# Performance work log

Hardware: AMD Instinct MI355X
Metric: run time of the kernel (lower is better)

The kernel has to match this reference:

```python
import jax, jax.numpy as jnp
import numpy as np

N_BONES = 8
NV = 14062
PARENTS = [-1, 0, 1, 2, 3, 4, 5, 6]  # kinematic chain


def rotvec_to_rotmat(rv):
    # rv: [..., 3] -> [..., 3, 3] via Rodrigues
    ang = jnp.sqrt(jnp.sum(rv * rv, axis=-1) + 1e-12)  # [...]
    k = rv / ang[..., None]
    kx, ky, kz = k[..., 0], k[..., 1], k[..., 2]
    z = jnp.zeros_like(kx)
    K = jnp.stack([
        jnp.stack([z, -kz, ky], -1),
        jnp.stack([kz, z, -kx], -1),
        jnp.stack([-ky, kx, z], -1)], -2)  # [...,3,3]
    s = jnp.sin(ang)[..., None, None]
    c = jnp.cos(ang)[..., None, None]
    I = jnp.eye(3, dtype=rv.dtype)
    return I + s * K + (1.0 - c) * (K @ K)


def bilinear_sample(img, gx, gy):
    # img: [H, W]; gx, gy: [B, Nv] normalized coords in [-1,1]
    # bilinear, border padding, align_corners=True (matches F.grid_sample)
    H, W = img.shape
    x = jnp.clip((gx + 1.0) * 0.5 * (W - 1), 0.0, W - 1.0)
    y = jnp.clip((gy + 1.0) * 0.5 * (H - 1), 0.0, H - 1.0)
    x0 = jnp.floor(x); y0 = jnp.floor(y)
    x0i = x0.astype(jnp.int32); y0i = y0.astype(jnp.int32)
    x1i = jnp.minimum(x0i + 1, W - 1); y1i = jnp.minimum(y0i + 1, H - 1)
    wx = x - x0; wy = y - y0
    v00 = img[y0i, x0i]; v01 = img[y0i, x1i]
    v10 = img[y1i, x0i]; v11 = img[y1i, x1i]
    return (v00 * (1 - wx) + v01 * wx) * (1 - wy) + (v10 * (1 - wx) + v11 * wx) * wy


def setup_inputs() -> dict:
    key = jax.random.key(0)
    ks = jax.random.split(key, 12)
    B = 256
    theta = jax.random.normal(ks[0], (B, N_BONES, 3), jnp.float32) * 0.3
    tau = jax.random.normal(ks[1], (B, 1), jnp.float32) * 0.1
    alpha = jax.random.uniform(ks[2], (B, 1), jnp.float32)
    bsw = jax.random.uniform(ks[3], (B, 55), jnp.float32)
    W = jax.random.uniform(ks[4], (N_BONES, NV), jnp.float32) + 1e-3
    W = W / W.sum(axis=0, keepdims=True)  # done in HACK.__init__
    T = jax.random.normal(ks[5], (NV, 3), jnp.float32)
    P = jax.random.normal(ks[6], (N_BONES, 3, 3, NV, 3), jnp.float32) * 0.01
    L = jax.random.uniform(ks[7], (1, 1, 256, 256), jnp.float32)
    ts = jax.random.normal(ks[8], (NV, 3), jnp.float32)
    # L2P: per-bone rigid transforms (rotation + small translation)
    rv = jax.random.normal(ks[9], (N_BONES, 3), jnp.float32) * 0.2
    R = rotvec_to_rotmat(rv)
    t = jax.random.normal(ks[10], (N_BONES, 3), jnp.float32) * 0.1
    L2P = jnp.tile(jnp.eye(4, dtype=jnp.float32), (N_BONES, 1, 1))
    L2P = L2P.at[:, :3, :3].set(R).at[:, :3, 3].set(t)
    E = jax.random.normal(ks[11], (55, NV, 3), jnp.float32) * 0.05
    uvgrid = jax.random.uniform(jax.random.fold_in(key, 99), (NV, 2), jnp.float32)
    return {"theta": theta, "tau": tau, "alpha": alpha, "bsw": bsw, "W": W,
            "T": T, "P": P, "L": L, "ts": ts, "L2P": L2P, "E": E, "uvgrid": uvgrid}


def reference(theta, tau, alpha, bsw, W, T, P, L, ts, L2P, E, uvgrid):
    B = theta.shape[0]
    R = rotvec_to_rotmat(theta)  # [B, Nb, 3, 3]
    # theta_matrix_zero: bone 0 subtracts itself (-> 0), others subtract I
    sub = jnp.concatenate([R[:, :1],
                           jnp.broadcast_to(jnp.eye(3, dtype=R.dtype), (B, N_BONES - 1, 3, 3))], axis=1)
    theta_zero = R - sub  # [B, Nb, 3, 3]
    # pose-corrective blendshapes: sum over (bone, i, j)
    P_theta = jnp.einsum('bnij,nijvk->bvk', theta_zero, P)  # [B, Nv, 3]

    # forward kinematics along chain: L2W_pose[i] = L2W_pose[parent] @ (L2P[i] @ local[i])
    local = jnp.tile(jnp.eye(4, dtype=R.dtype), (B, N_BONES, 1, 1))
    local = local.at[:, :, :3, :3].set(R)  # [B, Nb, 4, 4]
    mats = []
    for i in range(N_BONES):
        Ai = jnp.einsum('ij,bjk->bik', L2P[i], local[:, i])
        if PARENTS[i] >= 0:
            Ai = jnp.matmul(mats[PARENTS[i]], Ai)
        mats.append(Ai)
    L2W_pose = jnp.stack(mats, axis=1)  # [B, Nb, 4, 4]

    # rest-pose world-to-local (inverse bind matrices)
    rest = []
    for i in range(N_BONES):
        rest.append(L2P[i] if PARENTS[i] < 0 else rest[PARENTS[i]] @ L2P[i])
    W2L = jnp.linalg.inv(jnp.stack(rest))  # [Nb, 4, 4]

    W2L2pWs = jnp.einsum('bnij,njk->bnik', L2W_pose, W2L)  # [B, Nb, 4, 4]
    # skinning-weight contraction over bones -> per-vertex 4x4 transform
    M = jnp.einsum('bnij,nv->bvij', W2L2pWs, W)  # [B, Nv, 4, 4]

    # larynx displacement via grid_sample
    uv = uvgrid * 2.0 - 1.0  # [Nv, 2]
    gx = jnp.broadcast_to(uv[None, :, 0], (B, uv.shape[0]))
    gy = uv[None, :, 1] + tau * 2.0  # shift y by tau*2 (F.pad(tau*2,[1,0]))
    dist = bilinear_sample(L[0, 0], gx, gy)  # [B, Nv]
    L_tau = dist[:, :, None] * ts[None]  # [B, Nv, 3]

    T_theta = (T[None] + P_theta
               + jnp.einsum('bn,nvk->bvk', bsw, E)
               + L_tau * alpha[:, :, None])  # [B, Nv, 3]

    # homogeneous per-vertex 4x4 matvec, keep xyz
    T_transformed = (jnp.einsum('bvij,bvj->bvi', M[:, :, :3, :3], T_theta)
                     + M[:, :, :3, 3])
    return T_transformed
```

## Files before the change

kernel.cpp:

```cpp
#include <hip/hip_runtime.h>
#include <cmath>

#define NB     8
#define NVERT  14062
#define NV3    42186
#define BATCH  256
#define BB     32
#define NBT    16
#define KP     63
#define KE     55
#define KPAD   120
#define KT     8
#define NSTEP  15
#define VT     64

__device__ inline void mat4mul(const float* A, const float* B, float* C) {
#pragma unroll
  for (int i = 0; i < 4; i++)
#pragma unroll
    for (int j = 0; j < 4; j++) {
      float s = 0.f;
#pragma unroll
      for (int k = 0; k < 4; k++) s = fmaf(A[i*4+k], B[k*4+j], s);
      C[i*4+j] = s;
    }
}

__global__ void setup_kernel(const float* __restrict__ theta,
                             const float* __restrict__ bsw,
                             const float* __restrict__ L2P,
                             float* __restrict__ coef_t,
                             float* __restrict__ mats)
{
  int b = blockIdx.x * blockDim.x + threadIdx.x;
  if (b >= BATCH) return;

  float R[NB][9];
#pragma unroll
  for (int n = 0; n < NB; n++) {
    float rx = theta[(b*NB+n)*3+0];
    float ry = theta[(b*NB+n)*3+1];
    float rz = theta[(b*NB+n)*3+2];
    float ang = sqrtf(rx*rx + ry*ry + rz*rz + 1e-12f);
    float kx = rx/ang, ky = ry/ang, kz = rz/ang;
    float s = sinf(ang), c = cosf(ang);
    float K[9] = {0.f,-kz,ky,  kz,0.f,-kx,  -ky,kx,0.f};
    float K2[9];
#pragma unroll
    for (int i = 0; i < 3; i++)
#pragma unroll
      for (int j = 0; j < 3; j++) {
        float v = 0.f;
#pragma unroll
        for (int k = 0; k < 3; k++) v = fmaf(K[i*3+k], K[k*3+j], v);
        K2[i*3+j] = v;
      }
#pragma unroll
    for (int e = 0; e < 9; e++) {
      int i = e/3, j = e%3;
      R[n][e] = (i==j ? 1.f : 0.f) + s*K[e] + (1.f-c)*K2[e];
    }
  }

#pragma unroll
  for (int n = 1; n < NB; n++)
#pragma unroll
    for (int e = 0; e < 9; e++) {
      int i = e/3, j = e%3;
      coef_t[((n-1)*9+e)*BATCH + b] = R[n][e] - (i==j ? 1.f : 0.f);
    }
  for (int s2 = 0; s2 < KE; s2++)
    coef_t[(KP+s2)*BATCH + b] = bsw[b*KE + s2];
  coef_t[118*BATCH + b] = 0.f;
  coef_t[119*BATCH + b] = 0.f;

  float prevPose[16], prevRest[16];
#pragma unroll 1
  for (int n = 0; n < NB; n++) {
    float loc[16] = {R[n][0],R[n][1],R[n][2],0.f,
                     R[n][3],R[n][4],R[n][5],0.f,
                     R[n][6],R[n][7],R[n][8],0.f,
                     0.f,0.f,0.f,1.f};
    float A[16], pose[16], rest[16];
    mat4mul(&L2P[n*16], loc, A);
    if (n == 0) {
#pragma unroll
      for (int q = 0; q < 16; q++) { pose[q] = A[q]; rest[q] = L2P[q]; }
    } else {
      mat4mul(prevPose, A, pose);
      mat4mul(prevRest, &L2P[n*16], rest);
    }
    float w2l[16];
#pragma unroll
    for (int i = 0; i < 3; i++) {
#pragma unroll
      for (int j = 0; j < 3; j++) w2l[i*4+j] = rest[j*4+i];
      w2l[i*4+3] = -(rest[0*4+i]*rest[0*4+3] + rest[1*4+i]*rest[1*4+3] + rest[2*4+i]*rest[2*4+3]);
    }
    w2l[12]=0.f; w2l[13]=0.f; w2l[14]=0.f; w2l[15]=1.f;
    float skin[16];
    mat4mul(pose, w2l, skin);
#pragma unroll
    for (int i = 0; i < 3; i++)
#pragma unroll
      for (int j = 0; j < 4; j++)
        mats[(size_t)b*96 + n*12 + i*4 + j] = skin[i*4+j];
#pragma unroll
    for (int q = 0; q < 16; q++) { prevPose[q] = pose[q]; prevRest[q] = rest[q]; }
  }
}

__global__ __launch_bounds__(128) void fused_kernel(
    const float* __restrict__ P, const float* __restrict__ E,
    const float* __restrict__ coef_t, const float* __restrict__ matsg,
    const float* __restrict__ Wm, const float* __restrict__ T,
    const float* __restrict__ ts, const float* __restrict__ uvgrid,
    const float* __restrict__ Limg, const float* __restrict__ tau,
    const float* __restrict__ alpha, float* __restrict__ out)
{
  __shared__ float dlds[KT][VT*3];
  __shared__ float clds[KT][BB];
  __shared__ float mlds[BB][96];
  __shared__ float ta_s[BB], al_s[BB];

  int tid  = threadIdx.x;
  int lane = tid & 63;
  int wv   = tid >> 6;
  int bbase = blockIdx.x * BB;
  int vbase = blockIdx.y * VT;
  int v = vbase + lane;
  bool vok = v < NVERT;
  int vc = vok ? v : NVERT - 1;
  size_t vbase3 = (size_t)vbase * 3;
  bool full = (vbase + VT) <= NVERT;

#pragma unroll
  for (int r = 0; r < 6; r++) {
    int q = tid + r*128;
    int bb = q / 24, chunk = q - bb*24;
    float4 m = *reinterpret_cast<const float4*>(matsg + (size_t)(bbase+bb)*96 + chunk*4);
    *reinterpret_cast<float4*>(&mlds[bb][chunk*4]) = m;
  }
  if (tid < BB) { ta_s[tid] = tau[bbase+tid]; al_s[tid] = alpha[bbase+tid]; }

  auto loadD = [&](int step, float4 d[3]) {
    int c0 = step * KT;
#pragma unroll
    for (int r = 0; r < 3; r++) {
      int q = tid + r*128;
      int row = q / 48, posq = q - row*48;
      int c = c0 + row;
      const float* src = (c < KP) ? (P + (size_t)(9 + c)*NV3)
                                  : (E + (size_t)((c < KP+KE ? c : KP+KE-1) - KP)*NV3);
      if (full) {
        d[r] = *reinterpret_cast<const float4*>(src + vbase3 + posq*4);
      } else {
        float t0[4];
#pragma unroll
        for (int u = 0; u < 4; u++) {
          size_t idx = vbase3 + (size_t)posq*4 + u;
          if (idx >= NV3) idx = NV3 - 1;
          t0[u] = src[idx];
        }
        d[r] = make_float4(t0[0], t0[1], t0[2], t0[3]);
      }
    }
  };
  auto loadC = [&](int step, float4& c4) {
    if (tid < 64) {
      int row = tid >> 3, posq = tid & 7;
      c4 = *reinterpret_cast<const float4*>(
          coef_t + (size_t)(step*KT + row)*BATCH + bbase + posq*4);
    }
  };
  auto writeLDS = [&](float4 d[3], const float4& c4) {
#pragma unroll
    for (int r = 0; r < 3; r++)
      reinterpret_cast<float4*>(&dlds[0][0])[tid + r*128] = d[r];
    if (tid < 64) reinterpret_cast<float4*>(&clds[0][0])[tid] = c4;
  };

  float acc[NBT][3];
#pragma unroll
  for (int j = 0; j < NBT; j++) { acc[j][0]=0.f; acc[j][1]=0.f; acc[j][2]=0.f; }

  {
    float4 dpre[3]; float4 cpre;
    loadD(0, dpre); loadC(0, cpre);
    writeLDS(dpre, cpre);
  }
  __syncthreads();

  for (int step = 0; step < NSTEP; ++step) {
    float4 dpre[3]; float4 cpre;
    bool more = (step + 1 < NSTEP);
    if (more) { loadD(step+1, dpre); loadC(step+1, cpre); }
#pragma unroll
    for (int k = 0; k < KT; k++) {
      float d0 = dlds[k][lane*3+0];
      float d1 = dlds[k][lane*3+1];
      float d2 = dlds[k][lane*3+2];
      float4 ca = *reinterpret_cast<const float4*>(&clds[k][wv*NBT+0]);
      float4 cb = *reinterpret_cast<const float4*>(&clds[k][wv*NBT+4]);
      float4 cc = *reinterpret_cast<const float4*>(&clds[k][wv*NBT+8]);
      float4 cd = *reinterpret_cast<const float4*>(&clds[k][wv*NBT+12]);
      float cf[NBT] = {ca.x,ca.y,ca.z,ca.w, cb.x,cb.y,cb.z,cb.w,
                       cc.x,cc.y,cc.z,cc.w, cd.x,cd.y,cd.z,cd.w};
#pragma unroll
      for (int j = 0; j < NBT; j++) {
        acc[j][0] = fmaf(cf[j], d0, acc[j][0]);
        acc[j][1] = fmaf(cf[j], d1, acc[j][1]);
        acc[j][2] = fmaf(cf[j], d2, acc[j][2]);
      }
    }
    if (more) {
      __syncthreads();
      writeLDS(dpre, cpre);
      __syncthreads();
    }
  }

  float W8[NB];
#pragma unroll
  for (int n = 0; n < NB; n++) W8[n] = Wm[(size_t)n*NVERT + vc];
  float T0 = T[vc*3+0], T1 = T[vc*3+1], T2 = T[vc*3+2];
  float s0 = ts[vc*3+0], s1 = ts[vc*3+1], s2 = ts[vc*3+2];
  float u0 = uvgrid[vc*2+0], u1 = uvgrid[vc*2+1];

  float xc = fminf(fmaxf(u0*255.f, 0.f), 255.f);
  float xf = floorf(xc);
  int x0i = (int)xf;
  int x1i = min(x0i+1, 255);
  float wx = xc - xf;

#pragma unroll
  for (int j = 0; j < NBT; j++) {
    int bl = wv*NBT + j;
    float yc = fminf(fmaxf((u1 + ta_s[bl])*255.f, 0.f), 255.f);
    float yf = floorf(yc);
    int y0i = (int)yf;
    int y1i = min(y0i+1, 255);
    float wy = yc - yf;
    float v00 = Limg[y0i*256 + x0i], v01 = Limg[y0i*256 + x1i];
    float v10 = Limg[y1i*256 + x0i], v11 = Limg[y1i*256 + x1i];
    float dist = (v00*(1.f-wx) + v01*wx)*(1.f-wy) + (v10*(1.f-wx) + v11*wx)*wy;
    float da = dist * al_s[bl];

    float xv0 = acc[j][0] + T0 + da*s0;
    float xv1 = acc[j][1] + T1 + da*s1;
    float xv2 = acc[j][2] + T2 + da*s2;

    float o[3];
#pragma unroll
    for (int i = 0; i < 3; i++) {
      float c0=0.f, c1=0.f, c2=0.f, c3=0.f;
#pragma unroll
      for (int n = 0; n < NB; n++) {
        float4 m = *reinterpret_cast<const float4*>(&mlds[bl][n*12 + i*4]);
        float w = W8[n];
        c0 = fmaf(w, m.x, c0); c1 = fmaf(w, m.y, c1);
        c2 = fmaf(w, m.z, c2); c3 = fmaf(w, m.w, c3);
      }
      o[i] = fmaf(c0, xv0, fmaf(c1, xv1, fmaf(c2, xv2, c3)));
    }
    if (vok) {
      size_t off = (size_t)(bbase + bl)*NV3 + (size_t)v*3;
      out[off+0] = o[0];
      out[off+1] = o[1];
      out[off+2] = o[2];
    }
  }
}

extern "C" void kernel_launch(void* const* d_in, const int* in_sizes, int n_in,
                              void* d_out, int out_size, void* d_ws, size_t ws_size,
                              hipStream_t stream)
{
  const float* theta  = (const float*)d_in[0];
  const float* tau    = (const float*)d_in[1];
  const float* alpha  = (const float*)d_in[2];
  const float* bsw    = (const float*)d_in[3];
  const float* Wm     = (const float*)d_in[4];
  const float* T      = (const float*)d_in[5];
  const float* P      = (const float*)d_in[6];
  const float* L      = (const float*)d_in[7];
  const float* ts     = (const float*)d_in[8];
  const float* L2P    = (const float*)d_in[9];
  const float* E      = (const float*)d_in[10];
  const float* uvgrid = (const float*)d_in[11];
  float* out = (float*)d_out;

  float* coef_t = (float*)d_ws;
  float* mats   = coef_t + (size_t)KPAD * BATCH;

  setup_kernel<<<dim3(4), dim3(64), 0, stream>>>(theta, bsw, L2P, coef_t, mats);
  fused_kernel<<<dim3(BATCH/BB, (NVERT + VT - 1) / VT), dim3(128), 0, stream>>>(
      P, E, coef_t, mats, Wm, T, ts, uvgrid, L, tau, alpha, out);
}
```

Before: 221.6 us.

## Replace LDS-staged K loop with direct global loads and register double buffering

Drops the shared-memory staging of the P/E basis rows and coefficients, along with the two barriers per step. Each thread now loads its own vertex's three components and its 16 batch coefficients straight from global memory, with a two-row software pipeline held in registers. The block grows to 256 threads covering 64 batches, which halves the number of blocks along the batch axis. The cost is more redundant global and L2 traffic: the coefficients are loaded per thread, and the scalar stride-3 vertex loads coalesce less well than the earlier float4 loads.

After: 214.4 us. 1.03x faster.

```diff
diff --git a/kernel.cpp b/kernel.cpp
--- a/kernel.cpp
+++ b/kernel.cpp
@@ -5,13 +5,11 @@
 #define NVERT  14062
 #define NV3    42186
 #define BATCH  256
-#define BB     32
+#define BBLK   64
 #define NBT    16
 #define KP     63
 #define KE     55
-#define KPAD   120
-#define KT     8
-#define NSTEP  15
+#define KTOT   118
 #define VT     64
 
 __device__ inline void mat4mul(const float* A, const float* B, float* C) {
@@ -71,8 +69,6 @@
     }
   for (int s2 = 0; s2 < KE; s2++)
     coef_t[(KP+s2)*BATCH + b] = bsw[b*KE + s2];
-  coef_t[118*BATCH + b] = 0.f;
-  coef_t[119*BATCH + b] = 0.f;
 
   float prevPose[16], prevRest[16];
 #pragma unroll 1
@@ -110,7 +106,7 @@
   }
 }
 
-__global__ __launch_bounds__(128) void fused_kernel(
+__global__ __launch_bounds__(256) void fused_kernel(
     const float* __restrict__ P, const float* __restrict__ E,
     const float* __restrict__ coef_t, const float* __restrict__ matsg,
     const float* __restrict__ Wm, const float* __restrict__ T,
@@ -118,106 +114,80 @@
     const float* __restrict__ Limg, const float* __restrict__ tau,
     const float* __restrict__ alpha, float* __restrict__ out)
 {
-  __shared__ float dlds[KT][VT*3];
-  __shared__ float clds[KT][BB];
-  __shared__ float mlds[BB][96];
-  __shared__ float ta_s[BB], al_s[BB];
+  __shared__ float mlds[BBLK][96];
+  __shared__ float ta_s[BBLK], al_s[BBLK];
 
   int tid  = threadIdx.x;
   int lane = tid & 63;
   int wv   = tid >> 6;
-  int bbase = blockIdx.x * BB;
+  int bbase = blockIdx.x * BBLK;
   int vbase = blockIdx.y * VT;
   int v = vbase + lane;
   bool vok = v < NVERT;
   int vc = vok ? v : NVERT - 1;
-  size_t vbase3 = (size_t)vbase * 3;
-  bool full = (vbase + VT) <= NVERT;
+  size_t voff = (size_t)vc * 3;
 
 #pragma unroll
   for (int r = 0; r < 6; r++) {
-    int q = tid + r*128;
+    int q = tid + r*256;
     int bb = q / 24, chunk = q - bb*24;
-    float4 m = *reinterpret_cast<const float4*>(matsg + (size_t)(bbase+bb)*96 + chunk*4);
-    *reinterpret_cast<float4*>(&mlds[bb][chunk*4]) = m;
-  }
-  if (tid < BB) { ta_s[tid] = tau[bbase+tid]; al_s[tid] = alpha[bbase+tid]; }
-
-  auto loadD = [&](int step, float4 d[3]) {
-    int c0 = step * KT;
-#pragma unroll
-    for (int r = 0; r < 3; r++) {
-      int q = tid + r*128;
-      int row = q / 48, posq = q - row*48;
-      int c = c0 + row;
-      const float* src = (c < KP) ? (P + (size_t)(9 + c)*NV3)
-                                  : (E + (size_t)((c < KP+KE ? c : KP+KE-1) - KP)*NV3);
-      if (full) {
-        d[r] = *reinterpret_cast<const float4*>(src + vbase3 + posq*4);
-      } else {
-        float t0[4];
-#pragma unroll
-        for (int u = 0; u < 4; u++) {
-          size_t idx = vbase3 + (size_t)posq*4 + u;
-          if (idx >= NV3) idx = NV3 - 1;
-          t0[u] = src[idx];
-        }
-        d[r] = make_float4(t0[0], t0[1], t0[2], t0[3]);
-      }
-    }
-  };
-  auto loadC = [&](int step, float4& c4) {
-    if (tid < 64) {
-      int row = tid >> 3, posq = tid & 7;
-      c4 = *reinterpret_cast<const float4*>(
-          coef_t + (size_t)(step*KT + row)*BATCH + bbase + posq*4);
-    }
-  };
-  auto writeLDS = [&](float4 d[3], const float4& c4) {
-#pragma unroll
-    for (int r = 0; r < 3; r++)
-      reinterpret_cast<float4*>(&dlds[0][0])[tid + r*128] = d[r];
-    if (tid < 64) reinterpret_cast<float4*>(&clds[0][0])[tid] = c4;
-  };
+    *reinterpret_cast<float4*>(&mlds[bb][chunk*4]) =
+        *reinterpret_cast<const float4*>(matsg + (size_t)(bbase+bb)*96 + chunk*4);
+  }
+  if (tid < BBLK) { ta_s[tid] = tau[bbase+tid]; al_s[tid] = alpha[bbase+tid]; }
+  __syncthreads();
+
+  const float* Pb = P + (size_t)9 * NV3;
+  const float* cbase = coef_t + bbase + wv*NBT;
 
   float acc[NBT][3];
 #pragma unroll
   for (int j = 0; j < NBT; j++) { acc[j][0]=0.f; acc[j][1]=0.f; acc[j][2]=0.f; }
 
+  float dA0,dA1,dA2, dB0,dB1,dB2;
+  float4 cA0,cA1,cA2,cA3, cB0,cB1,cB2,cB3;
+
   {
-    float4 dpre[3]; float4 cpre;
-    loadD(0, dpre); loadC(0, cpre);
-    writeLDS(dpre, cpre);
-  }
-  __syncthreads();
-
-  for (int step = 0; step < NSTEP; ++step) {
-    float4 dpre[3]; float4 cpre;
-    bool more = (step + 1 < NSTEP);
-    if (more) { loadD(step+1, dpre); loadC(step+1, cpre); }
-#pragma unroll
-    for (int k = 0; k < KT; k++) {
-      float d0 = dlds[k][lane*3+0];
-      float d1 = dlds[k][lane*3+1];
-      float d2 = dlds[k][lane*3+2];
-      float4 ca = *reinterpret_cast<const float4*>(&clds[k][wv*NBT+0]);
-      float4 cb = *reinterpret_cast<const float4*>(&clds[k][wv*NBT+4]);
-      float4 cc = *reinterpret_cast<const float4*>(&clds[k][wv*NBT+8]);
-      float4 cd = *reinterpret_cast<const float4*>(&clds[k][wv*NBT+12]);
-      float cf[NBT] = {ca.x,ca.y,ca.z,ca.w, cb.x,cb.y,cb.z,cb.w,
-                       cc.x,cc.y,cc.z,cc.w, cd.x,cd.y,cd.z,cd.w};
-#pragma unroll
-      for (int j = 0; j < NBT; j++) {
-        acc[j][0] = fmaf(cf[j], d0, acc[j][0]);
-        acc[j][1] = fmaf(cf[j], d1, acc[j][1]);
-        acc[j][2] = fmaf(cf[j], d2, acc[j][2]);
-      }
-    }
-    if (more) {
-      __syncthreads();
-      writeLDS(dpre, cpre);
-      __syncthreads();
-    }
+    const float* rp = Pb + voff;
+    dA0 = rp[0]; dA1 = rp[1]; dA2 = rp[2];
+    const float* cp = cbase;
+    cA0 = *reinterpret_cast<const float4*>(cp+0);
+    cA1 = *reinterpret_cast<const float4*>(cp+4);
+    cA2 = *reinterpret_cast<const float4*>(cp+8);
+    cA3 = *reinterpret_cast<const float4*>(cp+12);
+  }
+
+#define FMA_ROW(D0,D1,D2,C0,C1,C2,C3)                                   \
+  {                                                                     \
+    float cf[NBT] = {C0.x,C0.y,C0.z,C0.w, C1.x,C1.y,C1.z,C1.w,          \
+                     C2.x,C2.y,C2.z,C2.w, C3.x,C3.y,C3.z,C3.w};         \
+    _Pragma("unroll")                                                   \
+    for (int j = 0; j < NBT; j++) {                                     \
+      acc[j][0] = fmaf(cf[j], D0, acc[j][0]);                           \
+      acc[j][1] = fmaf(cf[j], D1, acc[j][1]);                           \
+      acc[j][2] = fmaf(cf[j], D2, acc[j][2]);                           \
+    }                                                                   \
+  }
+
+#define LOAD_ROW(cn, D0,D1,D2, C0,C1,C2,C3)                             \
+  {                                                                     \
+    int c_ = (cn) <= (KTOT-1) ? (cn) : (KTOT-1);                        \
+    const float* rp = ((c_ < KP) ? (Pb + (size_t)c_*NV3)                \
+                                 : (E + (size_t)(c_-KP)*NV3)) + voff;   \
+    D0 = rp[0]; D1 = rp[1]; D2 = rp[2];                                 \
+    const float* cp = cbase + (size_t)c_*BATCH;                         \
+    C0 = *reinterpret_cast<const float4*>(cp+0);                        \
+    C1 = *reinterpret_cast<const float4*>(cp+4);                        \
+    C2 = *reinterpret_cast<const float4*>(cp+8);                        \
+    C3 = *reinterpret_cast<const float4*>(cp+12);                       \
+  }
+
+#pragma unroll 1
+  for (int c = 0; c < KTOT; c += 2) {
+    LOAD_ROW(c+1, dB0,dB1,dB2, cB0,cB1,cB2,cB3);
+    FMA_ROW(dA0,dA1,dA2, cA0,cA1,cA2,cA3);
+    LOAD_ROW(c+2, dA0,dA1,dA2, cA0,cA1,cA2,cA3);
+    FMA_ROW(dB0,dB1,dB2, cB0,cB1,cB2,cB3);
   }
 
   float W8[NB];
@@ -291,9 +261,9 @@
   float* out = (float*)d_out;
 
   float* coef_t = (float*)d_ws;
-  float* mats   = coef_t + (size_t)KPAD * BATCH;
+  float* mats   = coef_t + (size_t)KTOT * BATCH;
 
   setup_kernel<<<dim3(4), dim3(64), 0, stream>>>(theta, bsw, L2P, coef_t, mats);
-  fused_kernel<<<dim3(BATCH/BB, (NVERT + VT - 1) / VT), dim3(128), 0, stream>>>(
+  fused_kernel<<<dim3(BATCH/BBLK, (NVERT + VT - 1) / VT), dim3(256), 0, stream>>>(
       P, E, coef_t, mats, Wm, T, ts, uvgrid, L, tau, alpha, out);
 }
```
